# Kernel tuning notes

Measured on AMD Instinct MI355X. Metric: run time of the kernel, lower is better.

## Reference

```python
import jax, jax.numpy as jnp
import numpy as np

B, L, D, H, S, V, K = 2, 64, 1024, 512, 50000, 40000, 32
SLM_LOGITS_SCALE = 0.1
BN_EPS = 1e-5


def setup_inputs() -> dict:
    key = jax.random.key(0)
    ks = jax.random.split(key, 8)
    return {
        "cached_embeddings": jax.random.normal(ks[0], (B, L, D), dtype=jnp.float32),
        "bn_gamma": jnp.ones((L,), jnp.float32),
        "bn_beta": jnp.zeros((L,), jnp.float32),
        "W1": jax.random.normal(ks[1], (D, H), dtype=jnp.float32) * 0.02,
        "b1": jnp.zeros((H,), jnp.float32),
        "W2": jax.random.normal(ks[2], (H, S), dtype=jnp.float32) * 0.02,
        "b2": jnp.zeros((S,), jnp.float32),
        "W_slm": jax.random.normal(ks[3], (H, V), dtype=jnp.float32) * 0.02,
        "b_slm": jnp.zeros((V,), jnp.float32),
        # fixed degree k=32 with values 1/min(deg,k) = 1/32 (full-degree rows)
        "sl_weights": jnp.full((S, K), 1.0 / K, jnp.float32),
        "sl_idx": jax.random.randint(ks[4], (S, K), 0, V, dtype=jnp.int32),
    }


def reference(cached_embeddings, bn_gamma, bn_beta, W1, b1, W2, b2,
              W_slm, b_slm, sl_weights, sl_idx):
    x = cached_embeddings  # [B, L, D]
    # BatchNorm1d(win_size): channels are sequence positions; stats over (B, D)
    mean = jnp.mean(x, axis=(0, 2), keepdims=True)
    var = jnp.var(x, axis=(0, 2), keepdims=True)
    xn = (x - mean) * jax.lax.rsqrt(var + BN_EPS)
    x = xn * bn_gamma[None, :, None] + bn_beta[None, :, None]
    # DenseEncoder: hidden + sense logits
    h = jax.nn.relu(jnp.einsum('bld,dh->blh', x, W1) + b1)  # [B, L, H]
    y = jnp.einsum('blh,hs->bls', h, W2) + b2                # [B, L, S]
    # SLM head: lemma logits
    v = jnp.einsum('blh,hv->blv', h, W_slm) + b_slm          # [B, L, V]
    # sparse sense->lemma matmul == weighted bounded-degree gather-sum
    g = v[..., sl_idx]                                       # [B, L, S, K]
    slm_logits = jnp.einsum('blsk,sk->bls', g, sl_weights)   # [B, L, S]
    return y + slm_logits * SLM_LOGITS_SCALE
```

## Files before the change

### kernel.cpp

```cpp
#include <hip/hip_runtime.h>

#define LL 64
#define DD 1024
#define HH 512
#define SS 50000
#define VV 40000
#define KD 32
#define MM 128

typedef __bf16 bf16_t;
typedef __bf16 bf16x8 __attribute__((ext_vector_type(8)));
typedef __bf16 bf16x4 __attribute__((ext_vector_type(4)));
typedef __bf16 bf16x2 __attribute__((ext_vector_type(2)));
typedef float f32x4 __attribute__((ext_vector_type(4)));

__device__ __forceinline__ void async_ld16(const void* g, void* l) {
    __builtin_amdgcn_global_load_lds(
        (const __attribute__((address_space(1))) void*)g,
        (__attribute__((address_space(3))) void*)l, 16, 0, 0);
}

__global__ __launch_bounds__(256) void k_bn(const float* __restrict__ x,
        const float* __restrict__ gamma, const float* __restrict__ beta,
        bf16_t* __restrict__ xn) {
    int l = blockIdx.x;
    int t = threadIdx.x;
    int b = t >> 7;
    int d0 = (t & 127) << 3;
    const float* xp = x + (size_t)(b * LL + l) * DD + d0;
    float4 v0 = *(const float4*)xp;
    float4 v1 = *(const float4*)(xp + 4);
    float s  = v0.x + v0.y + v0.z + v0.w + v1.x + v1.y + v1.z + v1.w;
    float ss = v0.x*v0.x + v0.y*v0.y + v0.z*v0.z + v0.w*v0.w
             + v1.x*v1.x + v1.y*v1.y + v1.z*v1.z + v1.w*v1.w;
    #pragma unroll
    for (int off = 32; off > 0; off >>= 1) {
        s  += __shfl_xor(s, off);
        ss += __shfl_xor(ss, off);
    }
    __shared__ float red[8];
    int wv = t >> 6, ln = t & 63;
    if (ln == 0) { red[wv] = s; red[4 + wv] = ss; }
    __syncthreads();
    float tot  = red[0] + red[1] + red[2] + red[3];
    float tots = red[4] + red[5] + red[6] + red[7];
    float mean = tot * (1.0f / 2048.0f);
    float var  = tots * (1.0f / 2048.0f) - mean * mean;
    float rstd = rsqrtf(var + 1e-5f);
    float g   = gamma[l] * rstd;
    float ofs = beta[l] - mean * g;
    bf16x8 o;
    o[0] = (bf16_t)(v0.x * g + ofs);
    o[1] = (bf16_t)(v0.y * g + ofs);
    o[2] = (bf16_t)(v0.z * g + ofs);
    o[3] = (bf16_t)(v0.w * g + ofs);
    o[4] = (bf16_t)(v1.x * g + ofs);
    o[5] = (bf16_t)(v1.y * g + ofs);
    o[6] = (bf16_t)(v1.z * g + ofs);
    o[7] = (bf16_t)(v1.w * g + ofs);
    *(bf16x8*)(xn + (size_t)(b * LL + l) * DD + d0) = o;
}

__global__ __launch_bounds__(256) void k_gemm1(const bf16_t* __restrict__ xn,
        const float* __restrict__ W1, const float* __restrict__ b1,
        bf16_t* __restrict__ h) {
    int t = threadIdx.x;
    int wv = t >> 6, lane = t & 63;
    int c = lane & 15, q = lane >> 4;
    int tile = blockIdx.x * 4 + wv;
    int tm = tile >> 5, tn = tile & 31;
    int col = tn * 16 + c;
    f32x4 acc = {};
    for (int kk = 0; kk < DD; kk += 32) {
        bf16x8 afr = *(const bf16x8*)(xn + (size_t)(tm * 16 + c) * DD + kk + q * 8);
        bf16x8 bfr;
        #pragma unroll
        for (int j = 0; j < 8; ++j)
            bfr[j] = (bf16_t)W1[(size_t)(kk + q * 8 + j) * HH + col];
        acc = __builtin_amdgcn_mfma_f32_16x16x32_bf16(afr, bfr, acc, 0, 0, 0);
    }
    float bias = b1[col];
    #pragma unroll
    for (int r = 0; r < 4; ++r) {
        int m = tm * 16 + q * 4 + r;
        float v = acc[r] + bias;
        h[(size_t)m * HH + col] = (bf16_t)(v > 0.f ? v : 0.f);
    }
}

__global__ __launch_bounds__(256) void k_gemm_v(const bf16_t* __restrict__ h,
        const float* __restrict__ Wslm, const float* __restrict__ bslm,
        bf16_t* __restrict__ vT) {
    __shared__ float wt[2][32 * 64];
    int t = threadIdx.x;
    int wv = t >> 6, lane = t & 63;
    int c = lane & 15, q = lane >> 4;
    int nb = blockIdx.x * 64;
    int col = nb + wv * 16 + c;
    int r  = t >> 4, sg = t & 15;
    const float* g0 = Wslm + (size_t)r        * VV + nb + sg * 4;
    const float* g1 = Wslm + (size_t)(r + 16) * VV + nb + sg * 4;

    #define STAGE_V(buf, kk) do { \
        async_ld16(g0 + (size_t)(kk) * VV, &wt[buf][t * 4]); \
        async_ld16(g1 + (size_t)(kk) * VV, &wt[buf][(t + 256) * 4]); } while (0)

    STAGE_V(0, 0);
    f32x4 acc[8] = {};
    #pragma unroll 1
    for (int step = 0; step < 16; ++step) {
        int cur = step & 1;
        __syncthreads();
        if (step < 15) STAGE_V(cur ^ 1, (step + 1) * 32);
        int kk = step * 32;
        bf16x8 bfr;
        #pragma unroll
        for (int j = 0; j < 8; ++j)
            bfr[j] = (bf16_t)wt[cur][(q * 8 + j) * 64 + wv * 16 + c];
        #pragma unroll
        for (int ms = 0; ms < 8; ++ms) {
            bf16x8 afr = *(const bf16x8*)(h + (size_t)(ms * 16 + c) * HH + kk + q * 8);
            acc[ms] = __builtin_amdgcn_mfma_f32_16x16x32_bf16(afr, bfr, acc[ms], 0, 0, 0);
        }
    }
    float bias = bslm[col];
    #pragma unroll
    for (int ms = 0; ms < 8; ++ms) {
        bf16x4 o;
        #pragma unroll
        for (int rr = 0; rr < 4; ++rr) o[rr] = (bf16_t)(acc[ms][rr] + bias);
        *(bf16x4*)(vT + (size_t)col * MM + ms * 16 + q * 4) = o;
    }
    #undef STAGE_V
}

__global__ __launch_bounds__(256) void k_gather(const bf16_t* __restrict__ vT,
        const float* __restrict__ slw, const int* __restrict__ slidx,
        bf16_t* __restrict__ slm) {
    int t = threadIdx.x;
    int wv = t >> 6, lane = t & 63;
    int s = blockIdx.x * 4 + wv;
    int idv = slidx[(size_t)s * KD + (lane & 31)];
    float wgt = slw[(size_t)s * KD + (lane & 31)];
    unsigned int u[KD];
    #pragma unroll
    for (int k = 0; k < KD; ++k) {
        int id = __shfl(idv, k);
        u[k] = *(const unsigned int*)(vT + (size_t)id * MM + lane * 2);
    }
    float a0 = 0.f, a1 = 0.f;
    #pragma unroll
    for (int k = 0; k < KD; ++k) {
        float w = __shfl(wgt, k);
        a0 += w * __uint_as_float(u[k] << 16);
        a1 += w * __uint_as_float(u[k] & 0xffff0000u);
    }
    bf16x2 o;
    o[0] = (bf16_t)a0;
    o[1] = (bf16_t)a1;
    *(bf16x2*)(slm + (size_t)s * MM + lane * 2) = o;
}

__global__ __launch_bounds__(256) void k_gemm_y(const bf16_t* __restrict__ h,
        const float* __restrict__ W2, const float* __restrict__ b2,
        const bf16_t* __restrict__ slm, float* __restrict__ out) {
    __shared__ float wt[2][32 * 64];
    int t = threadIdx.x;
    int wv = t >> 6, lane = t & 63;
    int c = lane & 15, q = lane >> 4;
    int nb = blockIdx.x * 64;
    int col = nb + wv * 16 + c;
    int r  = t >> 4, sg = t & 15;
    int sgc = nb + sg * 4;
    bool ok = (sgc + 4 <= SS);
    const float* g0 = ok ? (W2 + (size_t)r        * SS + sgc) : W2;
    const float* g1 = ok ? (W2 + (size_t)(r + 16) * SS + sgc) : W2;

    #define STAGE_Y(buf, kk) do { \
        async_ld16(g0 + (size_t)(kk) * SS, &wt[buf][t * 4]); \
        async_ld16(g1 + (size_t)(kk) * SS, &wt[buf][(t + 256) * 4]); } while (0)

    STAGE_Y(0, 0);
    f32x4 acc[8] = {};
    #pragma unroll 1
    for (int step = 0; step < 16; ++step) {
        int cur = step & 1;
        __syncthreads();
        if (step < 15) STAGE_Y(cur ^ 1, (step + 1) * 32);
        int kk = step * 32;
        bf16x8 bfr;
        #pragma unroll
        for (int j = 0; j < 8; ++j)
            bfr[j] = (bf16_t)wt[cur][(q * 8 + j) * 64 + wv * 16 + c];
        #pragma unroll
        for (int ms = 0; ms < 8; ++ms) {
            bf16x8 afr = *(const bf16x8*)(h + (size_t)(ms * 16 + c) * HH + kk + q * 8);
            acc[ms] = __builtin_amdgcn_mfma_f32_16x16x32_bf16(afr, bfr, acc[ms], 0, 0, 0);
        }
    }
    if (col < SS) {
        float bias = b2[col];
        #pragma unroll
        for (int ms = 0; ms < 8; ++ms) {
            bf16x4 sv = *(const bf16x4*)(slm + (size_t)col * MM + ms * 16 + q * 4);
            #pragma unroll
            for (int rr = 0; rr < 4; ++rr) {
                int m = ms * 16 + q * 4 + rr;
                out[(size_t)m * SS + col] = acc[ms][rr] + bias + 0.1f * (float)sv[rr];
            }
        }
    }
    #undef STAGE_Y
}

extern "C" void kernel_launch(void* const* d_in, const int* in_sizes, int n_in,
                              void* d_out, int out_size, void* d_ws, size_t ws_size,
                              hipStream_t stream) {
    const float* x     = (const float*)d_in[0];
    const float* gamma = (const float*)d_in[1];
    const float* beta  = (const float*)d_in[2];
    const float* W1    = (const float*)d_in[3];
    const float* b1    = (const float*)d_in[4];
    const float* W2    = (const float*)d_in[5];
    const float* b2    = (const float*)d_in[6];
    const float* Wslm  = (const float*)d_in[7];
    const float* bslm  = (const float*)d_in[8];
    const float* slw   = (const float*)d_in[9];
    const int*   slidx = (const int*)d_in[10];
    float* out = (float*)d_out;

    char* ws = (char*)d_ws;
    bf16_t* xn  = (bf16_t*)ws;
    bf16_t* h   = (bf16_t*)(ws + 262144);
    bf16_t* vT  = (bf16_t*)(ws + 393216);
    bf16_t* slm = (bf16_t*)(ws + 10633216);

    k_bn    <<<64,    256, 0, stream>>>(x, gamma, beta, xn);
    k_gemm1 <<<64,    256, 0, stream>>>(xn, W1, b1, h);
    k_gemm_v<<<625,   256, 0, stream>>>(h, Wslm, bslm, vT);
    k_gather<<<12500, 256, 0, stream>>>(vT, slw, slidx, slm);
    k_gemm_y<<<782,   256, 0, stream>>>(h, W2, b2, slm, out);
}
```

Before: 353.8 us.

## Triple-buffer W and h tiles in LDS with vmcnt-based async pipelining

Both large GEMM kernels now stage the h activation tile into LDS alongside the weight tile, instead of reading h directly from global memory in every iteration. They use a three-stage ring buffer with explicit vmcnt waits and raw barriers, so loads can run two steps ahead of compute. The first GEMM is relaunched as 256 single-wave blocks instead of 64 four-wave blocks to spread it across more CUs. Costs are 48KB of LDS per block, which can lower occupancy, and hand-tuned waitcnt values that must match the number of loads issued per stage.

```diff
diff --git a/kernel.cpp b/kernel.cpp
--- a/kernel.cpp
+++ b/kernel.cpp
@@ -19,6 +19,8 @@
         (const __attribute__((address_space(1))) void*)g,
         (__attribute__((address_space(3))) void*)l, 16, 0, 0);
 }
+
+#define WAITV(N) asm volatile("s_waitcnt vmcnt(" #N ")" ::: "memory")
 
 __global__ __launch_bounds__(256) void k_bn(const float* __restrict__ x,
         const float* __restrict__ gamma, const float* __restrict__ beta,
@@ -61,13 +63,12 @@
     *(bf16x8*)(xn + (size_t)(b * LL + l) * DD + d0) = o;
 }
 
-__global__ __launch_bounds__(256) void k_gemm1(const bf16_t* __restrict__ xn,
+__global__ __launch_bounds__(64) void k_gemm1(const bf16_t* __restrict__ xn,
         const float* __restrict__ W1, const float* __restrict__ b1,
         bf16_t* __restrict__ h) {
-    int t = threadIdx.x;
-    int wv = t >> 6, lane = t & 63;
+    int lane = threadIdx.x & 63;
     int c = lane & 15, q = lane >> 4;
-    int tile = blockIdx.x * 4 + wv;
+    int tile = blockIdx.x;
     int tm = tile >> 5, tn = tile & 31;
     int col = tn * 16 + c;
     f32x4 acc = {};
@@ -91,38 +92,56 @@
 __global__ __launch_bounds__(256) void k_gemm_v(const bf16_t* __restrict__ h,
         const float* __restrict__ Wslm, const float* __restrict__ bslm,
         bf16_t* __restrict__ vT) {
-    __shared__ float wt[2][32 * 64];
+    __shared__ __align__(16) char smem[3][16384];
     int t = threadIdx.x;
     int wv = t >> 6, lane = t & 63;
     int c = lane & 15, q = lane >> 4;
     int nb = blockIdx.x * 64;
     int col = nb + wv * 16 + c;
     int r  = t >> 4, sg = t & 15;
-    const float* g0 = Wslm + (size_t)r        * VV + nb + sg * 4;
-    const float* g1 = Wslm + (size_t)(r + 16) * VV + nb + sg * 4;
+    const float* gw0 = Wslm + (size_t)r        * VV + nb + sg * 4;
+    const float* gw1 = Wslm + (size_t)(r + 16) * VV + nb + sg * 4;
+    int g0i = t, g1i = t + 256;
+    const bf16_t* gh0 = h + (size_t)(((g0i >> 6) << 4) + ((g0i >> 2) & 15)) * HH + (g0i & 3) * 8;
+    const bf16_t* gh1 = h + (size_t)(((g1i >> 6) << 4) + ((g1i >> 2) & 15)) * HH + (g1i & 3) * 8;
 
     #define STAGE_V(buf, kk) do { \
-        async_ld16(g0 + (size_t)(kk) * VV, &wt[buf][t * 4]); \
-        async_ld16(g1 + (size_t)(kk) * VV, &wt[buf][(t + 256) * 4]); } while (0)
-
-    STAGE_V(0, 0);
+        async_ld16(gw0 + (size_t)(kk) * VV, smem[buf] + (size_t)t * 16); \
+        async_ld16(gw1 + (size_t)(kk) * VV, smem[buf] + (size_t)(t + 256) * 16); \
+        async_ld16(gh0 + (kk), smem[buf] + 8192 + (size_t)t * 16); \
+        async_ld16(gh1 + (kk), smem[buf] + 8192 + (size_t)(t + 256) * 16); \
+    } while (0)
+
+    STAGE_V(0, 0); STAGE_V(1, 32); STAGE_V(2, 64);
     f32x4 acc[8] = {};
-    #pragma unroll 1
-    for (int step = 0; step < 16; ++step) {
-        int cur = step & 1;
-        __syncthreads();
-        if (step < 15) STAGE_V(cur ^ 1, (step + 1) * 32);
-        int kk = step * 32;
+
+    auto compute = [&](int cur) {
+        const float*  wb = (const float*)smem[cur];
+        const bf16_t* hb = (const bf16_t*)(smem[cur] + 8192);
         bf16x8 bfr;
         #pragma unroll
         for (int j = 0; j < 8; ++j)
-            bfr[j] = (bf16_t)wt[cur][(q * 8 + j) * 64 + wv * 16 + c];
+            bfr[j] = (bf16_t)wb[(q * 8 + j) * 64 + wv * 16 + c];
         #pragma unroll
         for (int ms = 0; ms < 8; ++ms) {
-            bf16x8 afr = *(const bf16x8*)(h + (size_t)(ms * 16 + c) * HH + kk + q * 8);
+            bf16x8 afr = *(const bf16x8*)(hb + (size_t)(ms * 64 + c * 4 + q) * 8);
             acc[ms] = __builtin_amdgcn_mfma_f32_16x16x32_bf16(afr, bfr, acc[ms], 0, 0, 0);
         }
-    }
+    };
+
+    #pragma unroll 1
+    for (int step = 0; step < 13; ++step) {
+        WAITV(8);
+        __builtin_amdgcn_s_barrier();
+        int cur = step % 3;
+        compute(cur);
+        __builtin_amdgcn_s_barrier();
+        STAGE_V(cur, (step + 3) * 32);
+    }
+    WAITV(8); __builtin_amdgcn_s_barrier(); compute(1);
+    WAITV(4); __builtin_amdgcn_s_barrier(); compute(2);
+    WAITV(0); __builtin_amdgcn_s_barrier(); compute(0);
+
     float bias = bslm[col];
     #pragma unroll
     for (int ms = 0; ms < 8; ++ms) {
@@ -164,7 +183,7 @@
 __global__ __launch_bounds__(256) void k_gemm_y(const bf16_t* __restrict__ h,
         const float* __restrict__ W2, const float* __restrict__ b2,
         const bf16_t* __restrict__ slm, float* __restrict__ out) {
-    __shared__ float wt[2][32 * 64];
+    __shared__ __align__(16) char smem[3][16384];
     int t = threadIdx.x;
     int wv = t >> 6, lane = t & 63;
     int c = lane & 15, q = lane >> 4;
@@ -173,31 +192,49 @@
     int r  = t >> 4, sg = t & 15;
     int sgc = nb + sg * 4;
     bool ok = (sgc + 4 <= SS);
-    const float* g0 = ok ? (W2 + (size_t)r        * SS + sgc) : W2;
-    const float* g1 = ok ? (W2 + (size_t)(r + 16) * SS + sgc) : W2;
+    const float* gw0 = ok ? (W2 + (size_t)r        * SS + sgc) : W2;
+    const float* gw1 = ok ? (W2 + (size_t)(r + 16) * SS + sgc) : W2;
+    int g0i = t, g1i = t + 256;
+    const bf16_t* gh0 = h + (size_t)(((g0i >> 6) << 4) + ((g0i >> 2) & 15)) * HH + (g0i & 3) * 8;
+    const bf16_t* gh1 = h + (size_t)(((g1i >> 6) << 4) + ((g1i >> 2) & 15)) * HH + (g1i & 3) * 8;
 
     #define STAGE_Y(buf, kk) do { \
-        async_ld16(g0 + (size_t)(kk) * SS, &wt[buf][t * 4]); \
-        async_ld16(g1 + (size_t)(kk) * SS, &wt[buf][(t + 256) * 4]); } while (0)
-
-    STAGE_Y(0, 0);
+        async_ld16(gw0 + (size_t)(kk) * SS, smem[buf] + (size_t)t * 16); \
+        async_ld16(gw1 + (size_t)(kk) * SS, smem[buf] + (size_t)(t + 256) * 16); \
+        async_ld16(gh0 + (kk), smem[buf] + 8192 + (size_t)t * 16); \
+        async_ld16(gh1 + (kk), smem[buf] + 8192 + (size_t)(t + 256) * 16); \
+    } while (0)
+
+    STAGE_Y(0, 0); STAGE_Y(1, 32); STAGE_Y(2, 64);
     f32x4 acc[8] = {};
-    #pragma unroll 1
-    for (int step = 0; step < 16; ++step) {
-        int cur = step & 1;
-        __syncthreads();
-        if (step < 15) STAGE_Y(cur ^ 1, (step + 1) * 32);
-        int kk = step * 32;
+
+    auto compute = [&](int cur) {
+        const float*  wb = (const float*)smem[cur];
+        const bf16_t* hb = (const bf16_t*)(smem[cur] + 8192);
         bf16x8 bfr;
         #pragma unroll
         for (int j = 0; j < 8; ++j)
-            bfr[j] = (bf16_t)wt[cur][(q * 8 + j) * 64 + wv * 16 + c];
+            bfr[j] = (bf16_t)wb[(q * 8 + j) * 64 + wv * 16 + c];
         #pragma unroll
         for (int ms = 0; ms < 8; ++ms) {
-            bf16x8 afr = *(const bf16x8*)(h + (size_t)(ms * 16 + c) * HH + kk + q * 8);
+            bf16x8 afr = *(const bf16x8*)(hb + (size_t)(ms * 64 + c * 4 + q) * 8);
             acc[ms] = __builtin_amdgcn_mfma_f32_16x16x32_bf16(afr, bfr, acc[ms], 0, 0, 0);
         }
-    }
+    };
+
+    #pragma unroll 1
+    for (int step = 0; step < 13; ++step) {
+        WAITV(8);
+        __builtin_amdgcn_s_barrier();
+        int cur = step % 3;
+        compute(cur);
+        __builtin_amdgcn_s_barrier();
+        STAGE_Y(cur, (step + 3) * 32);
+    }
+    WAITV(8); __builtin_amdgcn_s_barrier(); compute(1);
+    WAITV(4); __builtin_amdgcn_s_barrier(); compute(2);
+    WAITV(0); __builtin_amdgcn_s_barrier(); compute(0);
+
     if (col < SS) {
         float bias = b2[col];
         #pragma unroll
@@ -236,7 +273,7 @@
     bf16_t* slm = (bf16_t*)(ws + 10633216);
 
     k_bn    <<<64,    256, 0, stream>>>(x, gamma, beta, xn);
-    k_gemm1 <<<64,    256, 0, stream>>>(xn, W1, b1, h);
+    k_gemm1 <<<256,   64,  0, stream>>>(xn, W1, b1, h);
     k_gemm_v<<<625,   256, 0, stream>>>(h, Wslm, bslm, vT);
     k_gather<<<12500, 256, 0, stream>>>(vT, slw, slidx, slm);
     k_gemm_y<<<782,   256, 0, stream>>>(h, W2, b2, slm, out);
```

New measurement: 312.4 us. 1.13x faster.

## Pre-pack weights to bf16 MFMA layout in side blocks and pipeline GEMMs

Applied to the files above, without the earlier changes.

Converts W1, W_slm and W2 from fp32 into a bf16 layout pre-swizzled for MFMA fragments. The conversion runs in extra blocks attached to the preceding kernel, so it overlaps with the BN and GEMM work. The GEMMs now stream packed weights and activations through double-buffered LDS with async loads and a 128-column tile per block. The packing step reads all the fp32 weights and writes bf16 copies every call, which adds memory traffic in exchange for cheaper loads in the GEMM inner loops.

```diff
diff --git a/kernel.cpp b/kernel.cpp
--- a/kernel.cpp
+++ b/kernel.cpp
@@ -8,6 +8,10 @@
 #define KD 32
 #define MM 128
 
+#define NPAIR_W1 4
+#define NPAIR_V  313
+#define NPAIR_Y  391
+
 typedef __bf16 bf16_t;
 typedef __bf16 bf16x8 __attribute__((ext_vector_type(8)));
 typedef __bf16 bf16x4 __attribute__((ext_vector_type(4)));
@@ -20,10 +24,11 @@
         (__attribute__((address_space(3))) void*)l, 16, 0, 0);
 }
 
-__global__ __launch_bounds__(256) void k_bn(const float* __restrict__ x,
+#define WAITV(N) asm volatile("s_waitcnt vmcnt(" #N ")" ::: "memory")
+
+__device__ __forceinline__ void bn_body(int l, const float* __restrict__ x,
         const float* __restrict__ gamma, const float* __restrict__ beta,
         bf16_t* __restrict__ xn) {
-    int l = blockIdx.x;
     int t = threadIdx.x;
     int b = t >> 7;
     int d0 = (t & 127) << 3;
@@ -61,77 +66,141 @@
     *(bf16x8*)(xn + (size_t)(b * LL + l) * DD + d0) = o;
 }
 
-__global__ __launch_bounds__(256) void k_gemm1(const bf16_t* __restrict__ xn,
-        const float* __restrict__ W1, const float* __restrict__ b1,
-        bf16_t* __restrict__ h) {
-    int t = threadIdx.x;
-    int wv = t >> 6, lane = t & 63;
-    int c = lane & 15, q = lane >> 4;
-    int tile = blockIdx.x * 4 + wv;
-    int tm = tile >> 5, tn = tile & 31;
-    int col = tn * 16 + c;
-    f32x4 acc = {};
-    for (int kk = 0; kk < DD; kk += 32) {
-        bf16x8 afr = *(const bf16x8*)(xn + (size_t)(tm * 16 + c) * DD + kk + q * 8);
-        bf16x8 bfr;
-        #pragma unroll
-        for (int j = 0; j < 8; ++j)
-            bfr[j] = (bf16_t)W1[(size_t)(kk + q * 8 + j) * HH + col];
-        acc = __builtin_amdgcn_mfma_f32_16x16x32_bf16(afr, bfr, acc, 0, 0, 0);
-    }
-    float bias = b1[col];
-    #pragma unroll
-    for (int r = 0; r < 4; ++r) {
-        int m = tm * 16 + q * 4 + r;
-        float v = acc[r] + bias;
-        h[(size_t)m * HH + col] = (bf16_t)(v > 0.f ? v : 0.f);
-    }
-}
-
-__global__ __launch_bounds__(256) void k_gemm_v(const bf16_t* __restrict__ h,
-        const float* __restrict__ Wslm, const float* __restrict__ bslm,
-        bf16_t* __restrict__ vT) {
-    __shared__ float wt[2][32 * 64];
-    int t = threadIdx.x;
-    int wv = t >> 6, lane = t & 63;
-    int c = lane & 15, q = lane >> 4;
-    int nb = blockIdx.x * 64;
-    int col = nb + wv * 16 + c;
-    int r  = t >> 4, sg = t & 15;
-    const float* g0 = Wslm + (size_t)r        * VV + nb + sg * 4;
-    const float* g1 = Wslm + (size_t)(r + 16) * VV + nb + sg * 4;
-
-    #define STAGE_V(buf, kk) do { \
-        async_ld16(g0 + (size_t)(kk) * VV, &wt[buf][t * 4]); \
-        async_ld16(g1 + (size_t)(kk) * VV, &wt[buf][(t + 256) * 4]); } while (0)
-
-    STAGE_V(0, 0);
-    f32x4 acc[8] = {};
-    #pragma unroll 1
-    for (int step = 0; step < 16; ++step) {
-        int cur = step & 1;
-        __syncthreads();
-        if (step < 15) STAGE_V(cur ^ 1, (step + 1) * 32);
-        int kk = step * 32;
-        bf16x8 bfr;
-        #pragma unroll
-        for (int j = 0; j < 8; ++j)
-            bfr[j] = (bf16_t)wt[cur][(q * 8 + j) * 64 + wv * 16 + c];
+__device__ __forceinline__ void conv_body(const float* __restrict__ src,
+        bf16_t* __restrict__ dst, int p, int s, int scols, int kst) {
+    int t = threadIdx.x;
+    #pragma unroll
+    for (int half = 0; half < 2; ++half) {
+        int cid = t + half * 256;
+        int c = cid & 15, qq = (cid >> 4) & 3, wvv = (cid >> 6) & 3, ns = cid >> 8;
+        int col = p * 128 + ns * 64 + wvv * 16 + c;
+        int k0 = s * 32 + qq * 8;
+        bf16x8 o = {};
+        if (col < scols) {
+            #pragma unroll
+            for (int i = 0; i < 8; ++i)
+                o[i] = (bf16_t)src[(size_t)(k0 + i) * scols + col];
+        }
+        *(bf16x8*)(dst + ((size_t)(p * kst + s) * 512 + cid) * 8) = o;
+    }
+}
+
+__global__ __launch_bounds__(256) void k_prep(const float* __restrict__ x,
+        const float* __restrict__ gamma, const float* __restrict__ beta,
+        bf16_t* __restrict__ xn, const float* __restrict__ W1,
+        bf16_t* __restrict__ W1p) {
+    int bid = blockIdx.x;
+    if (bid < 64) { bn_body(bid, x, gamma, beta, xn); return; }
+    int u = bid - 64;
+    conv_body(W1, W1p, u >> 5, u & 31, HH, 32);
+}
+
+template<int KSTEPS>
+__device__ __forceinline__ void gemm_pipe(const bf16_t* __restrict__ A, int lda,
+        const bf16_t* __restrict__ Wp, int pair, char (*smem)[16384],
+        f32x4 (*acc)[2]) {
+    int t = threadIdx.x;
+    int row0 = ((t >> 6) << 4) + (t & 15);
+    int koff = ((t >> 4) & 3) * 8;
+    const bf16_t* a0 = A + (size_t)row0 * lda + koff;
+    const bf16_t* a1 = A + (size_t)(row0 + 64) * lda + koff;
+    const bf16_t* w0 = Wp + (size_t)pair * KSTEPS * 4096 + t * 8;
+
+    #define STAGE_P(buf, st) do { \
+        async_ld16(w0 + (size_t)(st) * 4096, smem[buf] + t * 16); \
+        async_ld16(w0 + (size_t)(st) * 4096 + 2048, smem[buf] + (t + 256) * 16); \
+        async_ld16(a0 + (st) * 32, smem[buf] + 8192 + t * 16); \
+        async_ld16(a1 + (st) * 32, smem[buf] + 8192 + (t + 256) * 16); } while (0)
+
+    STAGE_P(0, 0); STAGE_P(1, 1);
+    int lane = t & 63, wv = t >> 6;
+
+    auto comp = [&](int cur) {
+        const bf16_t* wl = (const bf16_t*)smem[cur];
+        const bf16_t* al = (const bf16_t*)(smem[cur] + 8192);
+        bf16x8 b0 = *(const bf16x8*)(wl + (size_t)(wv * 64 + lane) * 8);
+        bf16x8 b1 = *(const bf16x8*)(wl + (size_t)(256 + wv * 64 + lane) * 8);
         #pragma unroll
         for (int ms = 0; ms < 8; ++ms) {
-            bf16x8 afr = *(const bf16x8*)(h + (size_t)(ms * 16 + c) * HH + kk + q * 8);
-            acc[ms] = __builtin_amdgcn_mfma_f32_16x16x32_bf16(afr, bfr, acc[ms], 0, 0, 0);
-        }
-    }
-    float bias = bslm[col];
-    #pragma unroll
-    for (int ms = 0; ms < 8; ++ms) {
-        bf16x4 o;
+            bf16x8 afr = *(const bf16x8*)(al + (size_t)(ms * 64 + lane) * 8);
+            acc[ms][0] = __builtin_amdgcn_mfma_f32_16x16x32_bf16(afr, b0, acc[ms][0], 0, 0, 0);
+            acc[ms][1] = __builtin_amdgcn_mfma_f32_16x16x32_bf16(afr, b1, acc[ms][1], 0, 0, 0);
+        }
+    };
+
+    #pragma unroll 1
+    for (int st = 0; st < KSTEPS - 2; ++st) {
+        WAITV(4);
+        __builtin_amdgcn_s_barrier();
+        comp(st & 1);
+        __builtin_amdgcn_s_barrier();
+        STAGE_P(st & 1, st + 2);
+    }
+    WAITV(4); __builtin_amdgcn_s_barrier(); comp(0);
+    WAITV(0); __builtin_amdgcn_s_barrier(); comp(1);
+    #undef STAGE_P
+}
+
+__global__ __launch_bounds__(256) void k_gemm1p(const bf16_t* __restrict__ xn,
+        const bf16_t* __restrict__ W1p, const float* __restrict__ b1,
+        bf16_t* __restrict__ h, const float* __restrict__ Wslm,
+        bf16_t* __restrict__ Wvp) {
+    __shared__ __align__(16) char smem[2][16384];
+    int bid = blockIdx.x;
+    if (bid >= NPAIR_W1) {
+        int u = bid - NPAIR_W1;
+        conv_body(Wslm, Wvp, u >> 4, u & 15, VV, 16);
+        return;
+    }
+    f32x4 acc[8][2] = {};
+    gemm_pipe<32>(xn, DD, W1p, bid, smem, acc);
+    int t = threadIdx.x, lane = t & 63, wv = t >> 6;
+    int c = lane & 15, q = lane >> 4;
+    #pragma unroll
+    for (int ns = 0; ns < 2; ++ns) {
+        int col = bid * 128 + ns * 64 + wv * 16 + c;
+        float bias = b1[col];
         #pragma unroll
-        for (int rr = 0; rr < 4; ++rr) o[rr] = (bf16_t)(acc[ms][rr] + bias);
-        *(bf16x4*)(vT + (size_t)col * MM + ms * 16 + q * 4) = o;
-    }
-    #undef STAGE_V
+        for (int ms = 0; ms < 8; ++ms) {
+            #pragma unroll
+            for (int rr = 0; rr < 4; ++rr) {
+                int m = ms * 16 + q * 4 + rr;
+                float v = acc[ms][ns][rr] + bias;
+                h[(size_t)m * HH + col] = (bf16_t)(v > 0.f ? v : 0.f);
+            }
+        }
+    }
+}
+
+__global__ __launch_bounds__(256) void k_gemm_vp(const bf16_t* __restrict__ h,
+        const bf16_t* __restrict__ Wvp, const float* __restrict__ bslm,
+        bf16_t* __restrict__ vT, const float* __restrict__ W2,
+        bf16_t* __restrict__ W2p) {
+    __shared__ __align__(16) char smem[2][16384];
+    int bid = blockIdx.x;
+    if (bid >= NPAIR_V) {
+        int u = bid - NPAIR_V;
+        conv_body(W2, W2p, u >> 4, u & 15, SS, 16);
+        return;
+    }
+    f32x4 acc[8][2] = {};
+    gemm_pipe<16>(h, HH, Wvp, bid, smem, acc);
+    int t = threadIdx.x, lane = t & 63, wv = t >> 6;
+    int c = lane & 15, q = lane >> 4;
+    #pragma unroll
+    for (int ns = 0; ns < 2; ++ns) {
+        int col = bid * 128 + ns * 64 + wv * 16 + c;
+        if (col < VV) {
+            float bias = bslm[col];
+            #pragma unroll
+            for (int ms = 0; ms < 8; ++ms) {
+                bf16x4 o;
+                #pragma unroll
+                for (int rr = 0; rr < 4; ++rr) o[rr] = (bf16_t)(acc[ms][ns][rr] + bias);
+                *(bf16x4*)(vT + (size_t)col * MM + ms * 16 + q * 4) = o;
+            }
+        }
+    }
 }
 
 __global__ __launch_bounds__(256) void k_gather(const bf16_t* __restrict__ vT,
@@ -161,56 +230,31 @@
     *(bf16x2*)(slm + (size_t)s * MM + lane * 2) = o;
 }
 
-__global__ __launch_bounds__(256) void k_gemm_y(const bf16_t* __restrict__ h,
-        const float* __restrict__ W2, const float* __restrict__ b2,
+__global__ __launch_bounds__(256) void k_gemm_yp(const bf16_t* __restrict__ h,
+        const bf16_t* __restrict__ W2p, const float* __restrict__ b2,
         const bf16_t* __restrict__ slm, float* __restrict__ out) {
-    __shared__ float wt[2][32 * 64];
-    int t = threadIdx.x;
-    int wv = t >> 6, lane = t & 63;
+    __shared__ __align__(16) char smem[2][16384];
+    int bid = blockIdx.x;
+    f32x4 acc[8][2] = {};
+    gemm_pipe<16>(h, HH, W2p, bid, smem, acc);
+    int t = threadIdx.x, lane = t & 63, wv = t >> 6;
     int c = lane & 15, q = lane >> 4;
-    int nb = blockIdx.x * 64;
-    int col = nb + wv * 16 + c;
-    int r  = t >> 4, sg = t & 15;
-    int sgc = nb + sg * 4;
-    bool ok = (sgc + 4 <= SS);
-    const float* g0 = ok ? (W2 + (size_t)r        * SS + sgc) : W2;
-    const float* g1 = ok ? (W2 + (size_t)(r + 16) * SS + sgc) : W2;
-
-    #define STAGE_Y(buf, kk) do { \
-        async_ld16(g0 + (size_t)(kk) * SS, &wt[buf][t * 4]); \
-        async_ld16(g1 + (size_t)(kk) * SS, &wt[buf][(t + 256) * 4]); } while (0)
-
-    STAGE_Y(0, 0);
-    f32x4 acc[8] = {};
-    #pragma unroll 1
-    for (int step = 0; step < 16; ++step) {
-        int cur = step & 1;
-        __syncthreads();
-        if (step < 15) STAGE_Y(cur ^ 1, (step + 1) * 32);
-        int kk = step * 32;
-        bf16x8 bfr;
-        #pragma unroll
-        for (int j = 0; j < 8; ++j)
-            bfr[j] = (bf16_t)wt[cur][(q * 8 + j) * 64 + wv * 16 + c];
-        #pragma unroll
-        for (int ms = 0; ms < 8; ++ms) {
-            bf16x8 afr = *(const bf16x8*)(h + (size_t)(ms * 16 + c) * HH + kk + q * 8);
-            acc[ms] = __builtin_amdgcn_mfma_f32_16x16x32_bf16(afr, bfr, acc[ms], 0, 0, 0);
-        }
-    }
-    if (col < SS) {
-        float bias = b2[col];
-        #pragma unroll
-        for (int ms = 0; ms < 8; ++ms) {
-            bf16x4 sv = *(const bf16x4*)(slm + (size_t)col * MM + ms * 16 + q * 4);
-            #pragma unroll
-            for (int rr = 0; rr < 4; ++rr) {
-                int m = ms * 16 + q * 4 + rr;
-                out[(size_t)m * SS + col] = acc[ms][rr] + bias + 0.1f * (float)sv[rr];
+    #pragma unroll
+    for (int ns = 0; ns < 2; ++ns) {
+        int col = bid * 128 + ns * 64 + wv * 16 + c;
+        if (col < SS) {
+            float bias = b2[col];
+            #pragma unroll
+            for (int ms = 0; ms < 8; ++ms) {
+                bf16x4 sv = *(const bf16x4*)(slm + (size_t)col * MM + ms * 16 + q * 4);
+                #pragma unroll
+                for (int rr = 0; rr < 4; ++rr) {
+                    int m = ms * 16 + q * 4 + rr;
+                    out[(size_t)m * SS + col] = acc[ms][ns][rr] + bias + 0.1f * (float)sv[rr];
+                }
             }
         }
     }
-    #undef STAGE_Y
 }
 
 extern "C" void kernel_launch(void* const* d_in, const int* in_sizes, int n_in,
@@ -234,10 +278,13 @@
     bf16_t* h   = (bf16_t*)(ws + 262144);
     bf16_t* vT  = (bf16_t*)(ws + 393216);
     bf16_t* slm = (bf16_t*)(ws + 10633216);
-
-    k_bn    <<<64,    256, 0, stream>>>(x, gamma, beta, xn);
-    k_gemm1 <<<64,    256, 0, stream>>>(xn, W1, b1, h);
-    k_gemm_v<<<625,   256, 0, stream>>>(h, Wslm, bslm, vT);
-    k_gather<<<12500, 256, 0, stream>>>(vT, slw, slidx, slm);
-    k_gemm_y<<<782,   256, 0, stream>>>(h, W2, b2, slm, out);
-}
+    bf16_t* W1p = (bf16_t*)(ws + 23433216);
+    bf16_t* Wvp = (bf16_t*)(ws + 24481792);
+    bf16_t* W2p = (bf16_t*)(ws + 65507328);
+
+    k_prep   <<<64 + 128,          256, 0, stream>>>(x, gamma, beta, xn, W1, W1p);
+    k_gemm1p <<<NPAIR_W1 + 5008,   256, 0, stream>>>(xn, W1p, b1, h, Wslm, Wvp);
+    k_gemm_vp<<<NPAIR_V + 6256,    256, 0, stream>>>(h, Wvp, bslm, vT, W2, W2p);
+    k_gather <<<12500,             256, 0, stream>>>(vT, slw, slidx, slm);
+    k_gemm_yp<<<NPAIR_Y,           256, 0, stream>>>(h, W2p, b2, slm, out);
+}
```

New measurement: 330.9 us. -6.5%, faster.

## Load GEMM weights directly from global memory instead of async LDS staging

Applied to the files above, without the earlier changes.

The two large weight GEMMs (SLM head and sense logits) no longer stage fp32 weight tiles through double-buffered shared memory with async global-to-LDS loads and barriers. Each lane now reads its weight column straight from global memory into registers through a shared helper that unrolls the k loop by two. The first GEMM is also relaunched as 256 single-wave blocks instead of 64 four-wave blocks. This removes the LDS traffic and barrier synchronisation, but the strided per-lane global loads may coalesce less well and leave less latency hidden.

```diff
diff --git a/kernel.cpp b/kernel.cpp
--- a/kernel.cpp
+++ b/kernel.cpp
@@ -13,12 +13,6 @@
 typedef __bf16 bf16x4 __attribute__((ext_vector_type(4)));
 typedef __bf16 bf16x2 __attribute__((ext_vector_type(2)));
 typedef float f32x4 __attribute__((ext_vector_type(4)));
-
-__device__ __forceinline__ void async_ld16(const void* g, void* l) {
-    __builtin_amdgcn_global_load_lds(
-        (const __attribute__((address_space(1))) void*)g,
-        (__attribute__((address_space(3))) void*)l, 16, 0, 0);
-}
 
 __global__ __launch_bounds__(256) void k_bn(const float* __restrict__ x,
         const float* __restrict__ gamma, const float* __restrict__ beta,
@@ -61,16 +55,16 @@
     *(bf16x8*)(xn + (size_t)(b * LL + l) * DD + d0) = o;
 }
 
-__global__ __launch_bounds__(256) void k_gemm1(const bf16_t* __restrict__ xn,
+__global__ __launch_bounds__(64) void k_gemm1(const bf16_t* __restrict__ xn,
         const float* __restrict__ W1, const float* __restrict__ b1,
         bf16_t* __restrict__ h) {
-    int t = threadIdx.x;
-    int wv = t >> 6, lane = t & 63;
+    int lane = threadIdx.x & 63;
     int c = lane & 15, q = lane >> 4;
-    int tile = blockIdx.x * 4 + wv;
+    int tile = blockIdx.x;
     int tm = tile >> 5, tn = tile & 31;
     int col = tn * 16 + c;
     f32x4 acc = {};
+    #pragma unroll 2
     for (int kk = 0; kk < DD; kk += 32) {
         bf16x8 afr = *(const bf16x8*)(xn + (size_t)(tm * 16 + c) * DD + kk + q * 8);
         bf16x8 bfr;
@@ -88,41 +82,34 @@
     }
 }
 
+template<int WC, int KSTEPS>
+__device__ __forceinline__ void gemm_nolds(const bf16_t* __restrict__ A, int lda,
+        const float* __restrict__ Wc , int q, int c,
+        f32x4 (&acc)[8]) {
+    #pragma unroll 2
+    for (int st = 0; st < KSTEPS; ++st) {
+        const float* wp = Wc + (size_t)(st * 32 + q * 8) * WC;
+        bf16x8 bfr;
+        #pragma unroll
+        for (int j = 0; j < 8; ++j)
+            bfr[j] = (bf16_t)wp[(size_t)j * WC];
+        const bf16_t* ap = A + (size_t)c * lda + st * 32 + q * 8;
+        #pragma unroll
+        for (int ms = 0; ms < 8; ++ms) {
+            bf16x8 afr = *(const bf16x8*)(ap + (size_t)(ms * 16) * lda);
+            acc[ms] = __builtin_amdgcn_mfma_f32_16x16x32_bf16(afr, bfr, acc[ms], 0, 0, 0);
+        }
+    }
+}
+
 __global__ __launch_bounds__(256) void k_gemm_v(const bf16_t* __restrict__ h,
         const float* __restrict__ Wslm, const float* __restrict__ bslm,
         bf16_t* __restrict__ vT) {
-    __shared__ float wt[2][32 * 64];
-    int t = threadIdx.x;
-    int wv = t >> 6, lane = t & 63;
+    int t = threadIdx.x, wv = t >> 6, lane = t & 63;
     int c = lane & 15, q = lane >> 4;
-    int nb = blockIdx.x * 64;
-    int col = nb + wv * 16 + c;
-    int r  = t >> 4, sg = t & 15;
-    const float* g0 = Wslm + (size_t)r        * VV + nb + sg * 4;
-    const float* g1 = Wslm + (size_t)(r + 16) * VV + nb + sg * 4;
-
-    #define STAGE_V(buf, kk) do { \
-        async_ld16(g0 + (size_t)(kk) * VV, &wt[buf][t * 4]); \
-        async_ld16(g1 + (size_t)(kk) * VV, &wt[buf][(t + 256) * 4]); } while (0)
-
-    STAGE_V(0, 0);
+    int col = blockIdx.x * 64 + wv * 16 + c;
     f32x4 acc[8] = {};
-    #pragma unroll 1
-    for (int step = 0; step < 16; ++step) {
-        int cur = step & 1;
-        __syncthreads();
-        if (step < 15) STAGE_V(cur ^ 1, (step + 1) * 32);
-        int kk = step * 32;
-        bf16x8 bfr;
-        #pragma unroll
-        for (int j = 0; j < 8; ++j)
-            bfr[j] = (bf16_t)wt[cur][(q * 8 + j) * 64 + wv * 16 + c];
-        #pragma unroll
-        for (int ms = 0; ms < 8; ++ms) {
-            bf16x8 afr = *(const bf16x8*)(h + (size_t)(ms * 16 + c) * HH + kk + q * 8);
-            acc[ms] = __builtin_amdgcn_mfma_f32_16x16x32_bf16(afr, bfr, acc[ms], 0, 0, 0);
-        }
-    }
+    gemm_nolds<VV, 16>(h, HH, Wslm + col, q, c, acc);
     float bias = bslm[col];
     #pragma unroll
     for (int ms = 0; ms < 8; ++ms) {
@@ -131,7 +118,6 @@
         for (int rr = 0; rr < 4; ++rr) o[rr] = (bf16_t)(acc[ms][rr] + bias);
         *(bf16x4*)(vT + (size_t)col * MM + ms * 16 + q * 4) = o;
     }
-    #undef STAGE_V
 }
 
 __global__ __launch_bounds__(256) void k_gather(const bf16_t* __restrict__ vT,
@@ -164,40 +150,12 @@
 __global__ __launch_bounds__(256) void k_gemm_y(const bf16_t* __restrict__ h,
         const float* __restrict__ W2, const float* __restrict__ b2,
         const bf16_t* __restrict__ slm, float* __restrict__ out) {
-    __shared__ float wt[2][32 * 64];
-    int t = threadIdx.x;
-    int wv = t >> 6, lane = t & 63;
+    int t = threadIdx.x, wv = t >> 6, lane = t & 63;
     int c = lane & 15, q = lane >> 4;
-    int nb = blockIdx.x * 64;
-    int col = nb + wv * 16 + c;
-    int r  = t >> 4, sg = t & 15;
-    int sgc = nb + sg * 4;
-    bool ok = (sgc + 4 <= SS);
-    const float* g0 = ok ? (W2 + (size_t)r        * SS + sgc) : W2;
-    const float* g1 = ok ? (W2 + (size_t)(r + 16) * SS + sgc) : W2;
-
-    #define STAGE_Y(buf, kk) do { \
-        async_ld16(g0 + (size_t)(kk) * SS, &wt[buf][t * 4]); \
-        async_ld16(g1 + (size_t)(kk) * SS, &wt[buf][(t + 256) * 4]); } while (0)
-
-    STAGE_Y(0, 0);
+    int col = blockIdx.x * 64 + wv * 16 + c;
+    int lcol = col < SS ? col : SS - 1;
     f32x4 acc[8] = {};
-    #pragma unroll 1
-    for (int step = 0; step < 16; ++step) {
-        int cur = step & 1;
-        __syncthreads();
-        if (step < 15) STAGE_Y(cur ^ 1, (step + 1) * 32);
-        int kk = step * 32;
-        bf16x8 bfr;
-        #pragma unroll
-        for (int j = 0; j < 8; ++j)
-            bfr[j] = (bf16_t)wt[cur][(q * 8 + j) * 64 + wv * 16 + c];
-        #pragma unroll
-        for (int ms = 0; ms < 8; ++ms) {
-            bf16x8 afr = *(const bf16x8*)(h + (size_t)(ms * 16 + c) * HH + kk + q * 8);
-            acc[ms] = __builtin_amdgcn_mfma_f32_16x16x32_bf16(afr, bfr, acc[ms], 0, 0, 0);
-        }
-    }
+    gemm_nolds<SS, 16>(h, HH, W2 + lcol, q, c, acc);
     if (col < SS) {
         float bias = b2[col];
         #pragma unroll
@@ -210,7 +168,6 @@
             }
         }
     }
-    #undef STAGE_Y
 }
 
 extern "C" void kernel_launch(void* const* d_in, const int* in_sizes, int n_in,
@@ -236,7 +193,7 @@
     bf16_t* slm = (bf16_t*)(ws + 10633216);
 
     k_bn    <<<64,    256, 0, stream>>>(x, gamma, beta, xn);
-    k_gemm1 <<<64,    256, 0, stream>>>(xn, W1, b1, h);
+    k_gemm1 <<<256,   64,  0, stream>>>(xn, W1, b1, h);
     k_gemm_v<<<625,   256, 0, stream>>>(h, Wslm, bslm, vT);
     k_gather<<<12500, 256, 0, stream>>>(vT, slw, slidx, slm);
     k_gemm_y<<<782,   256, 0, stream>>>(h, W2, b2, slm, out);
```

New measurement: 376.1 us. 6.3% more time.
